# Kernel optimization log

Measured on AMD Instinct MI355X. Metric: run time of the kernel, lower is better.

## Reference

```python
import jax, jax.numpy as jnp
import numpy as np

N_NODES = 100000
N_EDGES = 1600000
IN_DIM, HID_DIM, OUT_DIM = 256, 64, 64
EPS = 1e-12  # F.normalize eps


def _gcn_conv(x, src, dst, norm, W, b, num_nodes):
    # PyG-style GCNConv: transform, then symmetric-normalized aggregation.
    h = x @ W                                   # [N, d_out]
    msg = norm[:, None] * h[src]                # [E+N, d_out] gathered messages
    out = jax.ops.segment_sum(msg, dst, num_segments=num_nodes)
    return out + b


def _l2_normalize(h):
    # F.normalize(h, p=2, dim=1)
    n = jnp.sqrt(jnp.sum(h * h, axis=-1, keepdims=True))
    return h / jnp.maximum(n, EPS)


def setup_inputs() -> dict:
    key = jax.random.key(0)
    ks = jax.random.split(key, 8)
    x = jax.random.normal(ks[0], (N_NODES, IN_DIM), dtype=jnp.float32)
    edge_index = jax.random.randint(ks[1], (2, N_EDGES), 0, N_NODES, dtype=jnp.int64)
    def glorot(k, fan_in, fan_out):
        s = np.sqrt(6.0 / (fan_in + fan_out)).astype(np.float32)
        return jax.random.uniform(k, (fan_in, fan_out), jnp.float32, -s, s)
    W1 = glorot(ks[2], IN_DIM, HID_DIM)
    W2 = glorot(ks[3], HID_DIM, HID_DIM)
    W3 = glorot(ks[4], HID_DIM, OUT_DIM)
    b1 = jnp.zeros((HID_DIM,), jnp.float32)
    b2 = jnp.zeros((HID_DIM,), jnp.float32)
    b3 = jnp.zeros((OUT_DIM,), jnp.float32)
    return {"x": x, "edge_index": edge_index,
            "W1": W1, "b1": b1, "W2": W2, "b2": b2, "W3": W3, "b3": b3}


def reference(x, edge_index, W1, b1, W2, b2, W3, b3):
    N = x.shape[0]
    # add self-loops and compute symmetric norm D^-1/2 A_hat D^-1/2
    loop = jnp.arange(N, dtype=edge_index.dtype)
    src = jnp.concatenate([edge_index[0], loop])
    dst = jnp.concatenate([edge_index[1], loop])
    deg = jax.ops.segment_sum(jnp.ones_like(src, dtype=x.dtype), dst, num_segments=N)
    dinv = jnp.where(deg > 0, jax.lax.rsqrt(jnp.maximum(deg, 1.0)), 0.0)
    norm = dinv[src] * dinv[dst]                # [E+N]

    # layer 1: conv -> relu -> (dropout p=0 = identity) -> L2-normalize
    h = jax.nn.relu(_gcn_conv(x, src, dst, norm, W1, b1, N))
    h = _l2_normalize(h)
    # layer 2
    h = jax.nn.relu(_gcn_conv(h, src, dst, norm, W2, b2, N))
    h = _l2_normalize(h)
    # final layer: plain conv (cast to float32, already float32)
    out = _gcn_conv(h, src, dst, norm, W3, b3, N)
    return out
```

## Files before the change

### kernel.cpp

```cpp
#include <hip/hip_runtime.h>
#include <hip/hip_bf16.h>
#include <math.h>

#define HID 64
#define KT 64

#define NBBITS 10
#define NBSZ 1024
#define P1_BMAX 128
#define P1_CH 4096
#define P1_CAP 96

typedef __attribute__((ext_vector_type(8))) short s16x8;
typedef __attribute__((ext_vector_type(4))) float f32x4;

static inline size_t align256(size_t x) { return (x + 255) & ~(size_t)255; }

__device__ inline void gld_lds16(const float* g, float* lds) {
  __builtin_amdgcn_global_load_lds((const __attribute__((address_space(1))) void*)g,
                                   (__attribute__((address_space(3))) void*)lds, 16, 0, 0);
}

__device__ inline unsigned short f2bf(float f) {
  unsigned u = __float_as_uint(f);
  return (unsigned short)((u + 0x7FFFu + ((u >> 16) & 1u)) >> 16);
}
__device__ inline float bf2f(unsigned short h) { return __uint_as_float(((unsigned)h) << 16); }
__device__ inline float bf_lo(unsigned int u) { return __uint_as_float(u << 16); }
__device__ inline float bf_hi(unsigned int u) { return __uint_as_float(u & 0xffff0000u); }


__global__ void count_dst_kernel(const int* __restrict__ dst, int* __restrict__ cnt, int E) {
  int e = blockIdx.x * blockDim.x + threadIdx.x;
  if (e < E) atomicAdd(&cnt[dst[e]], 1);
}

__global__ void dinv_kernel(const int* __restrict__ cnt, float* __restrict__ dinv, int N) {
  int i = blockIdx.x * blockDim.x + threadIdx.x;
  if (i < N) dinv[i] = rsqrtf((float)(cnt[i] + 1));
}


__global__ void bucket_count_kernel(const int* __restrict__ dst, int* __restrict__ bcnt,
                                    int E, int B) {
  __shared__ int sh[1024];
  for (int i = threadIdx.x; i < B; i += blockDim.x) sh[i] = 0;
  __syncthreads();
  for (int e = blockIdx.x * blockDim.x + threadIdx.x; e < E; e += gridDim.x * blockDim.x)
    atomicAdd(&sh[dst[e] >> NBBITS], 1);
  __syncthreads();
  for (int i = threadIdx.x; i < B; i += blockDim.x) {
    int v = sh[i];
    if (v) atomicAdd(&bcnt[i], v);
  }
}

__global__ __launch_bounds__(1024) void bucket_scan_kernel(const int* __restrict__ bcnt,
                                                           int* __restrict__ bbase,
                                                           int* __restrict__ gcur, int B) {
  __shared__ int sh[1024];
  int t = threadIdx.x;
  int v = (t < B) ? bcnt[t] : 0;
  sh[t] = v;
  __syncthreads();
  for (int off = 1; off < 1024; off <<= 1) {
    int u = (t >= off) ? sh[t - off] : 0;
    __syncthreads();
    sh[t] += u;
    __syncthreads();
  }
  if (t < B) {
    int ex = sh[t] - v;
    bbase[t] = ex;
    gcur[t] = ex;
  }
  if (t == 1023) bbase[B] = sh[1023];
}

__global__ __launch_bounds__(256) void bucketize_kernel(const int* __restrict__ src,
                                                        const int* __restrict__ dst,
                                                        int* __restrict__ gcur,
                                                        int* __restrict__ ebuck, int E) {
  __shared__ int cnt[P1_BMAX];
  __shared__ int lists[P1_BMAX * P1_CAP];
  int t = threadIdx.x;
  for (int i = t; i < P1_BMAX; i += 256) cnt[i] = 0;
  __syncthreads();
  int base_e = blockIdx.x * P1_CH;
#pragma unroll
  for (int u = 0; u < P1_CH / 256; ++u) {
    int e = base_e + u * 256 + t;
    if (e < E) {
      int s = src[e], d = dst[e];
      int bk = d >> NBBITS;
      int packed = (s << NBBITS) | (d & (NBSZ - 1));
      int p = atomicAdd(&cnt[bk], 1);
      if (p < P1_CAP) {
        lists[bk * P1_CAP + p] = packed;
      } else {
        int gp = atomicAdd(&gcur[bk], 1);
        ebuck[gp] = packed;
      }
    }
  }
  __syncthreads();
  int w = t >> 6, lane = t & 63;
  int bk = w * 32 + (lane & 31);
  int c = min(cnt[bk], P1_CAP);
  int mybase = 0;
  if (lane < 32 && c > 0) mybase = atomicAdd(&gcur[bk], c);
#pragma unroll 1
  for (int i = 0; i < 32; ++i) {
    int cb = __shfl(c, i);
    if (cb == 0) continue;
    int gb = __shfl(mybase, i);
    int bb = w * 32 + i;
    if (lane < cb) ebuck[gb + lane] = lists[bb * P1_CAP + lane];
    if (cb > 64 && lane < cb - 64) ebuck[gb + 64 + lane] = lists[bb * P1_CAP + 64 + lane];
  }
}

__global__ __launch_bounds__(1024) void bucket_sort_kernel(const int* __restrict__ ebuck,
                                                           const int* __restrict__ bbase,
                                                           int* __restrict__ rowptr,
                                                           int* __restrict__ epack,
                                                           float* __restrict__ dinv,
                                                           int N, int B, int E) {
  __shared__ int lcnt[NBSZ];
  __shared__ int lcur[NBSZ];
  int b = blockIdx.x;
  int t = threadIdx.x;
  int n0 = b << NBBITS;
  lcnt[t] = 0;
  __syncthreads();
  int e0 = bbase[b], e1 = bbase[b + 1];
  for (int i = e0 + t; i < e1; i += 1024) atomicAdd(&lcnt[ebuck[i] & (NBSZ - 1)], 1);
  __syncthreads();
  int v = lcnt[t];
  for (int off = 1; off < 1024; off <<= 1) {
    int u = (t >= off) ? lcnt[t - off] : 0;
    __syncthreads();
    lcnt[t] += u;
    __syncthreads();
  }
  int ex = lcnt[t] - v;
  int node = n0 + t;
  if (node < N) {
    rowptr[node] = e0 + ex;
    dinv[node] = rsqrtf((float)(v + 1));
  }
  if (b == B - 1 && t == 0) rowptr[N] = E;
  lcur[t] = e0 + ex;
  __syncthreads();
  for (int i = e0 + t; i < e1; i += 1024) {
    int pv = ebuck[i];
    int pos = atomicAdd(&lcur[pv & (NBSZ - 1)], 1);
    epack[pos] = ((unsigned)pv) >> NBBITS;
  }
}


__global__ void wprep_kernel(const float* __restrict__ W, unsigned short* __restrict__ Dh,
                             unsigned short* __restrict__ Dl) {
  int idx = blockIdx.x * 256 + threadIdx.x;
  int j = idx & 7, lane = (idx >> 3) & 63, ct = (idx >> 9) & 3, s = idx >> 11;
  int k = s * 32 + ((lane >> 4) << 3) + j;
  int col = ct * 16 + (lane & 15);
  float f = W[k * HID + col];
  unsigned short h = f2bf(f);
  Dh[idx] = h;
  Dl[idx] = f2bf(f - bf2f(h));
}


template <int K>
__global__ __launch_bounds__(256, 4) void gemm_mfma_kernel(
    const float* __restrict__ x, const unsigned short* __restrict__ Wh,
    const unsigned short* __restrict__ Wl, const float* __restrict__ dinv,
    unsigned short* __restrict__ out, int N) {
  constexpr int NS = K / 32;
  __shared__ float xs[2][64 * 32];
  const int t = threadIdx.x, lane = t & 63, w = t >> 6;
  const int g = lane >> 4, r15 = lane & 15;
  const int row0 = blockIdx.x * 64;
  const int arow = w * 16 + r15;
  f32x4 acc[4];
#pragma unroll
  for (int ct = 0; ct < 4; ++ct) acc[ct] = (f32x4){0.f, 0.f, 0.f, 0.f};

  auto stage = [&](int buf, int s) {
#pragma unroll
    for (int c = 0; c < 2; ++c) {
      int idx = c * 256 + t;
      int row = idx >> 3, gp = idx & 7;
      int gs = gp ^ (row & 7);
      int grow = min(row0 + row, N - 1);
      gld_lds16(x + (size_t)grow * K + s * 32 + gs * 4, &xs[buf][idx * 4]);
    }
  };
  stage(0, 0);
  for (int s = 0; s < NS; ++s) {
    __syncthreads();
    if (s + 1 < NS) stage((s + 1) & 1, s + 1);
    const float* xb = &xs[s & 1][arow * 32];
    float4 xv0 = *(const float4*)&xb[((2 * g) ^ (arow & 7)) * 4];
    float4 xv1 = *(const float4*)&xb[((2 * g + 1) ^ (arow & 7)) * 4];
    float xf[8] = {xv0.x, xv0.y, xv0.z, xv0.w, xv1.x, xv1.y, xv1.z, xv1.w};
    s16x8 xh, xl;
#pragma unroll
    for (int j = 0; j < 8; ++j) {
      unsigned short hb = f2bf(xf[j]);
      xh[j] = (short)hb;
      xl[j] = (short)f2bf(xf[j] - bf2f(hb));
    }
#pragma unroll
    for (int ct = 0; ct < 4; ++ct) {
      size_t o = (((size_t)(s * 4 + ct)) * 64 + lane) * 8;
      s16x8 wh = *(const s16x8*)&Wh[o];
      s16x8 wl = *(const s16x8*)&Wl[o];
      acc[ct] = __builtin_amdgcn_mfma_f32_16x16x32_bf16(wh, xh, acc[ct], 0, 0, 0);
      acc[ct] = __builtin_amdgcn_mfma_f32_16x16x32_bf16(wl, xh, acc[ct], 0, 0, 0);
      acc[ct] = __builtin_amdgcn_mfma_f32_16x16x32_bf16(wh, xl, acc[ct], 0, 0, 0);
    }
  }
  int row = row0 + arow;
  if (row < N) {
    float di = dinv[row];
    unsigned short* orow = out + (size_t)row * HID;
#pragma unroll
    for (int ct = 0; ct < 4; ++ct) {
      unsigned p0 = (unsigned)f2bf(di * acc[ct][0]) | ((unsigned)f2bf(di * acc[ct][1]) << 16);
      unsigned p1 = (unsigned)f2bf(di * acc[ct][2]) | ((unsigned)f2bf(di * acc[ct][3]) << 16);
      *(uint2*)&orow[ct * 16 + g * 4] = make_uint2(p0, p1);
    }
  }
}


__global__ __launch_bounds__(256) void agg_gemm_kernel(
    const int* __restrict__ rowptr, const int* __restrict__ ep,
    const float* __restrict__ dinv, const uint2* __restrict__ hin,
    const float* __restrict__ bias, const float* __restrict__ Wn,
    unsigned short* __restrict__ hout, int N) {
  __shared__ float Ws[64 * 64];
  __shared__ float vrow[16 * 65];
  const int t = threadIdx.x;
#pragma unroll
  for (int c = 0; c < 4; ++c) {
    int idx = c * 256 + t;
    gld_lds16(Wn + idx * 4, &Ws[idx * 4]);
  }
  const int w = t >> 6, lane = t & 63;
  const int q = lane >> 4, sub = lane & 15;
  const int lr = w * 4 + q;
  const int node = blockIdx.x * 16 + lr;
  const bool act = node < N;
  float di = 0.f;
  if (act) {
    int beg = rowptr[node];
    int end = rowptr[node + 1];
    uint2 su = hin[(size_t)node * 16 + sub];
    float a0 = bf_lo(su.x), a1 = bf_hi(su.x), a2 = bf_lo(su.y), a3 = bf_hi(su.y);
    int j = beg;
    for (; j + 8 <= end; j += 8) {
      int e[8];
      uint2 hv[8];
#pragma unroll
      for (int u = 0; u < 8; ++u) e[u] = ep[j + u];
#pragma unroll
      for (int u = 0; u < 8; ++u) hv[u] = hin[(size_t)e[u] * 16 + sub];
#pragma unroll
      for (int u = 0; u < 8; ++u) {
        a0 += bf_lo(hv[u].x); a1 += bf_hi(hv[u].x);
        a2 += bf_lo(hv[u].y); a3 += bf_hi(hv[u].y);
      }
    }
    for (; j < end; ++j) {
      uint2 hu = hin[(size_t)ep[j] * 16 + sub];
      a0 += bf_lo(hu.x); a1 += bf_hi(hu.x); a2 += bf_lo(hu.y); a3 += bf_hi(hu.y);
    }
    di = dinv[node];
    float4 b4 = *(const float4*)&bias[sub * 4];
    float4 v;
    v.x = fmaxf(fmaf(di, a0, b4.x), 0.f);
    v.y = fmaxf(fmaf(di, a1, b4.y), 0.f);
    v.z = fmaxf(fmaf(di, a2, b4.z), 0.f);
    v.w = fmaxf(fmaf(di, a3, b4.w), 0.f);
    float ss = v.x * v.x + v.y * v.y + v.z * v.z + v.w * v.w;
#pragma unroll
    for (int off = 8; off; off >>= 1) ss += __shfl_xor(ss, off, 64);
    float inv = 1.f / fmaxf(sqrtf(ss), 1e-12f);
    v.x *= inv; v.y *= inv; v.z *= inv; v.w *= inv;
    *(float4*)&vrow[lr * 65 + sub * 4] = v;
  }
  __syncthreads();
  if (act) {
    float4 o = make_float4(0.f, 0.f, 0.f, 0.f);
#pragma unroll 8
    for (int f = 0; f < 64; ++f) {
      float vf = vrow[lr * 65 + f];
      float4 wf = *(const float4*)&Ws[f * 64 + sub * 4];
      o.x = fmaf(vf, wf.x, o.x);
      o.y = fmaf(vf, wf.y, o.y);
      o.z = fmaf(vf, wf.z, o.z);
      o.w = fmaf(vf, wf.w, o.w);
    }
    unsigned p0 = (unsigned)f2bf(di * o.x) | ((unsigned)f2bf(di * o.y) << 16);
    unsigned p1 = (unsigned)f2bf(di * o.z) | ((unsigned)f2bf(di * o.w) << 16);
    *(uint2*)&hout[(size_t)node * HID + sub * 4] = make_uint2(p0, p1);
  }
}


template <bool RELU_NORM>
__global__ void agg_kernel(const int* __restrict__ rowptr, const int* __restrict__ ep,
                           const float* __restrict__ dinv, const uint2* __restrict__ h64,
                           const float* __restrict__ bias, float* __restrict__ out, int N) {
  int grp = (blockIdx.x * blockDim.x + threadIdx.x) >> 6;
  int lane = threadIdx.x & 63;
  int q = lane >> 4;
  int sub = lane & 15;
  int node = grp * 4 + q;
  if (node >= N) return;
  int beg = rowptr[node];
  int end = rowptr[node + 1];
  uint2 su = h64[(size_t)node * 16 + sub];
  float a0 = bf_lo(su.x), a1 = bf_hi(su.x), a2 = bf_lo(su.y), a3 = bf_hi(su.y);
  int j = beg;
  for (; j + 8 <= end; j += 8) {
    int e[8];
    uint2 hv[8];
#pragma unroll
    for (int u = 0; u < 8; ++u) e[u] = ep[j + u];
#pragma unroll
    for (int u = 0; u < 8; ++u) hv[u] = h64[(size_t)e[u] * 16 + sub];
#pragma unroll
    for (int u = 0; u < 8; ++u) {
      a0 += bf_lo(hv[u].x); a1 += bf_hi(hv[u].x);
      a2 += bf_lo(hv[u].y); a3 += bf_hi(hv[u].y);
    }
  }
  for (; j < end; ++j) {
    uint2 hu = h64[(size_t)ep[j] * 16 + sub];
    a0 += bf_lo(hu.x); a1 += bf_hi(hu.x); a2 += bf_lo(hu.y); a3 += bf_hi(hu.y);
  }
  float di = dinv[node];
  float4 b4 = *(const float4*)&bias[sub * 4];
  float4 v;
  v.x = fmaf(di, a0, b4.x); v.y = fmaf(di, a1, b4.y);
  v.z = fmaf(di, a2, b4.z); v.w = fmaf(di, a3, b4.w);
  if (RELU_NORM) {
    v.x = fmaxf(v.x, 0.f); v.y = fmaxf(v.y, 0.f);
    v.z = fmaxf(v.z, 0.f); v.w = fmaxf(v.w, 0.f);
    float ss = v.x * v.x + v.y * v.y + v.z * v.z + v.w * v.w;
#pragma unroll
    for (int off = 8; off; off >>= 1) ss += __shfl_xor(ss, off, 64);
    float inv = 1.f / fmaxf(sqrtf(ss), 1e-12f);
    v.x *= inv; v.y *= inv; v.z *= inv; v.w *= inv;
  }
  *(float4*)&out[(size_t)node * HID + sub * 4] = v;
}


template <int K, typename OT>
__global__ __launch_bounds__(256, 4) void gemm_kernel(const float* __restrict__ x,
                                                      const float* __restrict__ W,
                                                      OT* __restrict__ out, int N) {
  __shared__ float Xs[64 * KT];
  __shared__ float Ws[KT * 64];
  const int t = threadIdx.x;
  const int lane = t & 63;
  const int w = t >> 6;
  const int rg = lane >> 4;
  const int cg = lane & 15;
  const int row0 = blockIdx.x * 64;
  float4 acc[4];
#pragma unroll
  for (int r = 0; r < 4; ++r) acc[r] = make_float4(0.f, 0.f, 0.f, 0.f);

  for (int k0 = 0; k0 < K; k0 += KT) {
    if (k0) __syncthreads();
    const float* Wg = W + (size_t)k0 * HID;
#pragma unroll
    for (int c = 0; c < 4; ++c) {
      int idx = c * 256 + t;
      gld_lds16(Wg + idx * 4, &Ws[idx * 4]);
      int srow = idx >> 4;
      int sg = (idx & 15) ^ ((srow >> 2) & 3);
      int grow = min(row0 + srow, N - 1);
      gld_lds16(x + (size_t)grow * K + k0 + (sg << 2), &Xs[idx * 4]);
    }
    __syncthreads();
    const int rbase = w * 16 + rg * 4;
#pragma unroll 4
    for (int kb = 0; kb < KT / 4; ++kb) {
      float4 wq0 = *(const float4*)&Ws[(4 * kb + 0) * HID + cg * 4];
      float4 wq1 = *(const float4*)&Ws[(4 * kb + 1) * HID + cg * 4];
      float4 wq2 = *(const float4*)&Ws[(4 * kb + 2) * HID + cg * 4];
      float4 wq3 = *(const float4*)&Ws[(4 * kb + 3) * HID + cg * 4];
      const int sg = (kb ^ rg) << 2;
#pragma unroll
      for (int r = 0; r < 4; ++r) {
        float4 xv = *(const float4*)&Xs[(rbase + r) * KT + sg];
        acc[r].x = fmaf(xv.w, wq3.x, fmaf(xv.z, wq2.x, fmaf(xv.y, wq1.x, fmaf(xv.x, wq0.x, acc[r].x))));
        acc[r].y = fmaf(xv.w, wq3.y, fmaf(xv.z, wq2.y, fmaf(xv.y, wq1.y, fmaf(xv.x, wq0.y, acc[r].y))));
        acc[r].z = fmaf(xv.w, wq3.z, fmaf(xv.z, wq2.z, fmaf(xv.y, wq1.z, fmaf(xv.x, wq0.z, acc[r].z))));
        acc[r].w = fmaf(xv.w, wq3.w, fmaf(xv.z, wq2.w, fmaf(xv.y, wq1.w, fmaf(xv.x, wq0.w, acc[r].w))));
      }
    }
  }
#pragma unroll
  for (int r = 0; r < 4; ++r) {
    int row = row0 + w * 16 + rg * 4 + r;
    if (row < N) {
      OT* o = out + (size_t)row * HID + cg * 4;
      o[0] = (OT)acc[r].x; o[1] = (OT)acc[r].y; o[2] = (OT)acc[r].z; o[3] = (OT)acc[r].w;
    }
  }
}


__global__ void init_agg_kernel(const float* __restrict__ dinv, const float* __restrict__ h,
                                const float* __restrict__ bias, float* __restrict__ out, int N) {
  int t = blockIdx.x * blockDim.x + threadIdx.x;
  int i = t >> 6, f = t & 63;
  if (i >= N) return;
  float di = dinv[i];
  out[t] = di * di * h[t] + bias[f];
}

__global__ void edge_atomic_kernel(const int* __restrict__ src, const int* __restrict__ dst,
                                   const float* __restrict__ dinv, const float* __restrict__ h,
                                   float* __restrict__ out, int E) {
  int t = blockIdx.x * blockDim.x + threadIdx.x;
  int e = t >> 6;
  if (e >= E) return;
  int f = t & 63;
  int s = src[e], d = dst[e];
  atomicAdd(&out[(size_t)d * HID + f], dinv[s] * dinv[d] * h[(size_t)s * HID + f]);
}

__global__ void relu_norm_kernel(float* __restrict__ hbuf, int N) {
  int t = blockIdx.x * blockDim.x + threadIdx.x;
  int i = t >> 6;
  if (i >= N) return;
  float v = fmaxf(hbuf[t], 0.f);
  float ss = v * v;
#pragma unroll
  for (int off = 32; off; off >>= 1) ss += __shfl_xor(ss, off, 64);
  hbuf[t] = v / fmaxf(sqrtf(ss), 1e-12f);
}


extern "C" void kernel_launch(void* const* d_in, const int* in_sizes, int n_in,
                              void* d_out, int out_size, void* d_ws, size_t ws_size,
                              hipStream_t stream) {
  const float* x  = (const float*)d_in[0];
  const int*   ei = (const int*)d_in[1];
  const float* W1 = (const float*)d_in[2];
  const float* b1 = (const float*)d_in[3];
  const float* W2 = (const float*)d_in[4];
  const float* b2 = (const float*)d_in[5];
  const float* W3 = (const float*)d_in[6];
  const float* b3 = (const float*)d_in[7];
  float* out = (float*)d_out;

  const int IN = in_sizes[2] / HID;
  const int N  = in_sizes[0] / IN;
  const int E  = in_sizes[1] / 2;
  const int* srcI = ei;
  const int* dstI = ei + E;
  const int B = (N + NBSZ - 1) >> NBBITS;

  char* w = (char*)d_ws;
  size_t off = 0;
  auto alloc = [&](size_t bytes) { void* p = w + off; off = align256(off + bytes); return p; };
  float* A      = (float*)alloc((size_t)N * HID * 4);
  float* dinv   = (float*)alloc((size_t)N * 4);
  int*   cnt    = (int*)alloc((size_t)N * 4);
  size_t base_need = off;
  int*   rowptr = (int*)alloc((size_t)(N + 1) * 4);
  int*   epack  = (int*)alloc((size_t)E * 4);
  int*   bbase  = (int*)alloc(1032 * 4);
  int*   gcur   = (int*)alloc(1024 * 4);
  int*   bcnt   = (int*)alloc(1024 * 4);
  unsigned short* W1h = (unsigned short*)alloc(16384 * 2);
  unsigned short* W1l = (unsigned short*)alloc(16384 * 2);
  size_t csr_need = off;

  if (base_need > ws_size) return;
  const bool use_csr = (csr_need <= ws_size) && (B <= P1_BMAX) &&
                       ((size_t)E <= (size_t)N * HID) && (N <= (1 << 20));
  unsigned short* hsA = (unsigned short*)A;
  unsigned short* hsB = hsA + (size_t)N * HID;
  int* ebuck = (int*)A;

  const int blkE    = (E + 255) / 256;
  const int blkN    = (N + 255) / 256;
  const int blkRow  = (N + 63) / 64;
  const int blkWave = (N * 64 + 255) / 256;
  const int blkAgg  = ((size_t)((N + 3) / 4) * 64 + 255) / 256;
  const int blkFuse = (N + 15) / 16;
  const int blkEF   = ((size_t)E * 64 + 255) / 256;
  const int blkBkt  = (E + P1_CH - 1) / P1_CH;

  if (use_csr) {
    hipMemsetAsync(bcnt, 0, 1024 * 4, stream);
    wprep_kernel<<<64, 256, 0, stream>>>(W1, W1h, W1l);
    bucket_count_kernel<<<256, 256, 0, stream>>>(dstI, bcnt, E, B);
    bucket_scan_kernel<<<1, 1024, 0, stream>>>(bcnt, bbase, gcur, B);
    bucketize_kernel<<<blkBkt, 256, 0, stream>>>(srcI, dstI, gcur, ebuck, E);
    bucket_sort_kernel<<<B, 1024, 0, stream>>>(ebuck, bbase, rowptr, epack, dinv, N, B, E);

    gemm_mfma_kernel<256><<<blkRow, 256, 0, stream>>>(x, W1h, W1l, dinv, hsA, N);
    agg_gemm_kernel<<<blkFuse, 256, 0, stream>>>(rowptr, epack, dinv, (const uint2*)hsA,
                                                 b1, W2, hsB, N);
    agg_gemm_kernel<<<blkFuse, 256, 0, stream>>>(rowptr, epack, dinv, (const uint2*)hsB,
                                                 b2, W3, hsA, N);
    agg_kernel<false><<<blkAgg, 256, 0, stream>>>(rowptr, epack, dinv, (const uint2*)hsA,
                                                  b3, out, N);
  } else {
    hipMemsetAsync(cnt, 0, (size_t)N * 4, stream);
    count_dst_kernel<<<blkE, 256, 0, stream>>>(dstI, cnt, E);
    dinv_kernel<<<blkN, 256, 0, stream>>>(cnt, dinv, N);

    gemm_kernel<256><<<blkRow, 256, 0, stream>>>(x, W1, A, N);
    init_agg_kernel<<<blkWave, 256, 0, stream>>>(dinv, A, b1, out, N);
    edge_atomic_kernel<<<blkEF, 256, 0, stream>>>(srcI, dstI, dinv, A, out, E);
    relu_norm_kernel<<<blkWave, 256, 0, stream>>>(out, N);

    gemm_kernel<64><<<blkRow, 256, 0, stream>>>(out, W2, A, N);
    init_agg_kernel<<<blkWave, 256, 0, stream>>>(dinv, A, b2, out, N);
    edge_atomic_kernel<<<blkEF, 256, 0, stream>>>(srcI, dstI, dinv, A, out, E);
    relu_norm_kernel<<<blkWave, 256, 0, stream>>>(out, N);

    gemm_kernel<64><<<blkRow, 256, 0, stream>>>(out, W3, A, N);
    init_agg_kernel<<<blkWave, 256, 0, stream>>>(dinv, A, b3, out, N);
    edge_atomic_kernel<<<blkEF, 256, 0, stream>>>(srcI, dstI, dinv, A, out, E);
  }
}
```

Before: 381.6 us.

## Use smaller dst buckets, fuse weight prep with bucket count, drop agg_gemm block barrier

Dst buckets shrink from 1024 to 512 nodes, so 196 buckets are sorted by 512-thread blocks, and the per-block LDS lists hold 44 entries per bucket. The weight-split prep and bucket counting now run in one launch with different blocks doing each job. In agg_gemm the post-aggregation block barrier is removed by giving each wave its own vrow staging slot, with a single barrier kept after the async weight load. This aims to cut launch count, raise sort parallelism and reduce sync stalls. The smaller LDS capacity means more edges spill to global atomics.

Measured after the change: 382.3 us. About the same (+0.2%).

```diff
diff --git a/kernel.cpp b/kernel.cpp
--- a/kernel.cpp
+++ b/kernel.cpp
@@ -5,11 +5,11 @@
 #define HID 64
 #define KT 64
 
-#define NBBITS 10
-#define NBSZ 1024
-#define P1_BMAX 128
+#define NBBITS 9
+#define NBSZ 512
+#define P1_BMAX 256
 #define P1_CH 4096
-#define P1_CAP 96
+#define P1_CAP 44
 
 typedef __attribute__((ext_vector_type(8))) short s16x8;
 typedef __attribute__((ext_vector_type(4))) float f32x4;
@@ -41,19 +41,34 @@
 }
 
 
-__global__ void bucket_count_kernel(const int* __restrict__ dst, int* __restrict__ bcnt,
-                                    int E, int B) {
+__global__ void prep_kernel(const float* __restrict__ W, unsigned short* __restrict__ Dh,
+                            unsigned short* __restrict__ Dl, const int* __restrict__ dst,
+                            int* __restrict__ bcnt, int E, int B) {
   __shared__ int sh[1024];
-  for (int i = threadIdx.x; i < B; i += blockDim.x) sh[i] = 0;
-  __syncthreads();
-  for (int e = blockIdx.x * blockDim.x + threadIdx.x; e < E; e += gridDim.x * blockDim.x)
-    atomicAdd(&sh[dst[e] >> NBBITS], 1);
-  __syncthreads();
-  for (int i = threadIdx.x; i < B; i += blockDim.x) {
-    int v = sh[i];
-    if (v) atomicAdd(&bcnt[i], v);
-  }
-}
+  int b = blockIdx.x, t = threadIdx.x;
+  if (b < 64) {
+    int idx = b * 256 + t;
+    int j = idx & 7, lane = (idx >> 3) & 63, ct = (idx >> 9) & 3, s = idx >> 11;
+    int k = s * 32 + ((lane >> 4) << 3) + j;
+    int col = ct * 16 + (lane & 15);
+    float f = W[k * HID + col];
+    unsigned short h = f2bf(f);
+    Dh[idx] = h;
+    Dl[idx] = f2bf(f - bf2f(h));
+  } else {
+    int cb = b - 64, nb = gridDim.x - 64;
+    for (int i = t; i < B; i += 256) sh[i] = 0;
+    __syncthreads();
+    for (int e = cb * 256 + t; e < E; e += nb * 256)
+      atomicAdd(&sh[dst[e] >> NBBITS], 1);
+    __syncthreads();
+    for (int i = t; i < B; i += 256) {
+      int v = sh[i];
+      if (v) atomicAdd(&bcnt[i], v);
+    }
+  }
+}
+
 
 __global__ __launch_bounds__(1024) void bucket_scan_kernel(const int* __restrict__ bcnt,
                                                            int* __restrict__ bbase,
@@ -76,6 +91,7 @@
   }
   if (t == 1023) bbase[B] = sh[1023];
 }
+
 
 __global__ __launch_bounds__(256) void bucketize_kernel(const int* __restrict__ src,
                                                         const int* __restrict__ dst,
@@ -105,27 +121,27 @@
   }
   __syncthreads();
   int w = t >> 6, lane = t & 63;
-  int bk = w * 32 + (lane & 31);
+  int bk = w * 64 + lane;
   int c = min(cnt[bk], P1_CAP);
   int mybase = 0;
-  if (lane < 32 && c > 0) mybase = atomicAdd(&gcur[bk], c);
+  if (c > 0) mybase = atomicAdd(&gcur[bk], c);
 #pragma unroll 1
-  for (int i = 0; i < 32; ++i) {
+  for (int i = 0; i < 64; ++i) {
     int cb = __shfl(c, i);
     if (cb == 0) continue;
     int gb = __shfl(mybase, i);
-    int bb = w * 32 + i;
+    int bb = w * 64 + i;
     if (lane < cb) ebuck[gb + lane] = lists[bb * P1_CAP + lane];
-    if (cb > 64 && lane < cb - 64) ebuck[gb + 64 + lane] = lists[bb * P1_CAP + 64 + lane];
-  }
-}
-
-__global__ __launch_bounds__(1024) void bucket_sort_kernel(const int* __restrict__ ebuck,
-                                                           const int* __restrict__ bbase,
-                                                           int* __restrict__ rowptr,
-                                                           int* __restrict__ epack,
-                                                           float* __restrict__ dinv,
-                                                           int N, int B, int E) {
+  }
+}
+
+
+__global__ __launch_bounds__(512) void bucket_sort_kernel(const int* __restrict__ ebuck,
+                                                          const int* __restrict__ bbase,
+                                                          int* __restrict__ rowptr,
+                                                          int* __restrict__ epack,
+                                                          float* __restrict__ dinv,
+                                                          int N, int B, int E) {
   __shared__ int lcnt[NBSZ];
   __shared__ int lcur[NBSZ];
   int b = blockIdx.x;
@@ -134,10 +150,10 @@
   lcnt[t] = 0;
   __syncthreads();
   int e0 = bbase[b], e1 = bbase[b + 1];
-  for (int i = e0 + t; i < e1; i += 1024) atomicAdd(&lcnt[ebuck[i] & (NBSZ - 1)], 1);
+  for (int i = e0 + t; i < e1; i += NBSZ) atomicAdd(&lcnt[ebuck[i] & (NBSZ - 1)], 1);
   __syncthreads();
   int v = lcnt[t];
-  for (int off = 1; off < 1024; off <<= 1) {
+  for (int off = 1; off < NBSZ; off <<= 1) {
     int u = (t >= off) ? lcnt[t - off] : 0;
     __syncthreads();
     lcnt[t] += u;
@@ -152,24 +168,11 @@
   if (b == B - 1 && t == 0) rowptr[N] = E;
   lcur[t] = e0 + ex;
   __syncthreads();
-  for (int i = e0 + t; i < e1; i += 1024) {
+  for (int i = e0 + t; i < e1; i += NBSZ) {
     int pv = ebuck[i];
     int pos = atomicAdd(&lcur[pv & (NBSZ - 1)], 1);
     epack[pos] = ((unsigned)pv) >> NBBITS;
   }
-}
-
-
-__global__ void wprep_kernel(const float* __restrict__ W, unsigned short* __restrict__ Dh,
-                             unsigned short* __restrict__ Dl) {
-  int idx = blockIdx.x * 256 + threadIdx.x;
-  int j = idx & 7, lane = (idx >> 3) & 63, ct = (idx >> 9) & 3, s = idx >> 11;
-  int k = s * 32 + ((lane >> 4) << 3) + j;
-  int col = ct * 16 + (lane & 15);
-  float f = W[k * HID + col];
-  unsigned short h = f2bf(f);
-  Dh[idx] = h;
-  Dl[idx] = f2bf(f - bf2f(h));
 }
 
 
@@ -243,20 +246,20 @@
     const float* __restrict__ bias, const float* __restrict__ Wn,
     unsigned short* __restrict__ hout, int N) {
   __shared__ float Ws[64 * 64];
-  __shared__ float vrow[16 * 65];
+  __shared__ float vrow[4][4 * 68];
   const int t = threadIdx.x;
 #pragma unroll
   for (int c = 0; c < 4; ++c) {
     int idx = c * 256 + t;
     gld_lds16(Wn + idx * 4, &Ws[idx * 4]);
   }
+  __syncthreads();
   const int w = t >> 6, lane = t & 63;
   const int q = lane >> 4, sub = lane & 15;
-  const int lr = w * 4 + q;
-  const int node = blockIdx.x * 16 + lr;
-  const bool act = node < N;
+  const int node = blockIdx.x * 16 + w * 4 + q;
+  float4 v = make_float4(0.f, 0.f, 0.f, 0.f);
   float di = 0.f;
-  if (act) {
+  if (node < N) {
     int beg = rowptr[node];
     int end = rowptr[node + 1];
     uint2 su = hin[(size_t)node * 16 + sub];
@@ -281,7 +284,6 @@
     }
     di = dinv[node];
     float4 b4 = *(const float4*)&bias[sub * 4];
-    float4 v;
     v.x = fmaxf(fmaf(di, a0, b4.x), 0.f);
     v.y = fmaxf(fmaf(di, a1, b4.y), 0.f);
     v.z = fmaxf(fmaf(di, a2, b4.z), 0.f);
@@ -291,14 +293,13 @@
     for (int off = 8; off; off >>= 1) ss += __shfl_xor(ss, off, 64);
     float inv = 1.f / fmaxf(sqrtf(ss), 1e-12f);
     v.x *= inv; v.y *= inv; v.z *= inv; v.w *= inv;
-    *(float4*)&vrow[lr * 65 + sub * 4] = v;
-  }
-  __syncthreads();
-  if (act) {
+  }
+  *(float4*)&vrow[w][q * 68 + sub * 4] = v;
+  if (node < N) {
     float4 o = make_float4(0.f, 0.f, 0.f, 0.f);
 #pragma unroll 8
     for (int f = 0; f < 64; ++f) {
-      float vf = vrow[lr * 65 + f];
+      float vf = vrow[w][q * 68 + f];
       float4 wf = *(const float4*)&Ws[f * 64 + sub * 4];
       o.x = fmaf(vf, wf.x, o.x);
       o.y = fmaf(vf, wf.y, o.y);
@@ -489,7 +490,7 @@
   size_t csr_need = off;
 
   if (base_need > ws_size) return;
-  const bool use_csr = (csr_need <= ws_size) && (B <= P1_BMAX) &&
+  const bool use_csr = (csr_need <= ws_size) && (B <= P1_BMAX) && (B <= 1024) &&
                        ((size_t)E <= (size_t)N * HID) && (N <= (1 << 20));
   unsigned short* hsA = (unsigned short*)A;
   unsigned short* hsB = hsA + (size_t)N * HID;
@@ -506,11 +507,10 @@
 
   if (use_csr) {
     hipMemsetAsync(bcnt, 0, 1024 * 4, stream);
-    wprep_kernel<<<64, 256, 0, stream>>>(W1, W1h, W1l);
-    bucket_count_kernel<<<256, 256, 0, stream>>>(dstI, bcnt, E, B);
+    prep_kernel<<<320, 256, 0, stream>>>(W1, W1h, W1l, dstI, bcnt, E, B);
     bucket_scan_kernel<<<1, 1024, 0, stream>>>(bcnt, bbase, gcur, B);
     bucketize_kernel<<<blkBkt, 256, 0, stream>>>(srcI, dstI, gcur, ebuck, E);
-    bucket_sort_kernel<<<B, 1024, 0, stream>>>(ebuck, bbase, rowptr, epack, dinv, N, B, E);
+    bucket_sort_kernel<<<B, NBSZ, 0, stream>>>(ebuck, bbase, rowptr, epack, dinv, N, B, E);
 
     gemm_mfma_kernel<256><<<blkRow, 256, 0, stream>>>(x, W1h, W1l, dinv, hsA, N);
     agg_gemm_kernel<<<blkFuse, 256, 0, stream>>>(rowptr, epack, dinv, (const uint2*)hsA,
```
